# Kernel tuning notes

Hardware: AMD Instinct MI355X
Metric: run time of the kernel (lower is better)

Reference implementation:

```python
import jax, jax.numpy as jnp
import numpy as np


def setup_inputs() -> dict:
    key = jax.random.key(0)
    ks = jax.random.split(key, 5)
    B, C_in, C_out, H, W, k = 16, 64, 64, 256, 256, 16
    scale = 1.0 / (C_in * C_out)
    return {
        "u": jax.random.normal(ks[0], (B, C_in, H, W), dtype=jnp.float32),
        "W_pos_re": scale * jax.random.normal(ks[1], (C_in, C_out, k, k), dtype=jnp.float32),
        "W_pos_im": scale * jax.random.normal(ks[2], (C_in, C_out, k, k), dtype=jnp.float32),
        "W_neg_re": scale * jax.random.normal(ks[3], (C_in, C_out, k, k), dtype=jnp.float32),
        "W_neg_im": scale * jax.random.normal(ks[4], (C_in, C_out, k, k), dtype=jnp.float32),
    }


def reference(u, W_pos_re, W_pos_im, W_neg_re, W_neg_im):
    B, C_in, H, W = u.shape
    C_out = W_pos_re.shape[1]
    k = W_pos_re.shape[2]
    W_half = W // 2 + 1
    k_h = min(k, H // 2)
    k_w = min(k, W_half)

    R_pos = (W_pos_re + 1j * W_pos_im)[:, :, :k_h, :k_w]  # (C_in, C_out, k_h, k_w)
    R_neg = (W_neg_re + 1j * W_neg_im)[:, :, :k_h, :k_w]

    u_hat = jnp.fft.rfft2(u, norm="ortho")  # (B, C_in, H, W_half) complex

    # spectral multiply on retained modes only
    top = jnp.einsum("bchw,cohw->bohw", u_hat[:, :, :k_h, :k_w], R_pos)
    bot = jnp.einsum("bchw,cohw->bohw", u_hat[:, :, H - k_h:, :k_w], R_neg)

    v_hat = jnp.zeros((B, C_out, H, W_half), dtype=u_hat.dtype)
    v_hat = v_hat.at[:, :, :k_h, :k_w].set(top)
    v_hat = v_hat.at[:, :, H - k_h:, :k_w].set(bot)

    return jnp.fft.irfft2(v_hat, s=(H, W), norm="ortho")  # (B, C_out, H, W) real
```

## Files before the change

### kernel.cpp

```cpp
#include <hip/hip_runtime.h>


#define B_    16
#define H_    256
#define W_    256

#define OFF_CT 0
#define OFF_ST 256
#define OFF_RP 512
#define RP_SZ  (4096*512*2)
#define OFF_U  (OFF_RP + RP_SZ)
#define U_SZ   (512*1024*2)
#define OFF_V  (OFF_U + U_SZ)

#define UTP   260

typedef const __attribute__((address_space(1))) void g_void;
typedef __attribute__((address_space(3))) void l_void;

__device__ __forceinline__ void load_lds16(const float* g, float* l) {
    __builtin_amdgcn_global_load_lds((g_void*)g, (l_void*)l, 16, 0, 0);
}

__global__ void k_twiddle(float* __restrict__ ws) {
    int t = threadIdx.x;
    double a = 2.0 * 3.14159265358979323846 * (double)t / 256.0;
    ws[OFF_CT + t] = (float)cos(a);
    ws[OFF_ST + t] = (float)sin(a);
}

__global__ __launch_bounds__(256) void k_repack(const float* __restrict__ wpr,
                                                const float* __restrict__ wpi,
                                                const float* __restrict__ wnr,
                                                const float* __restrict__ wni,
                                                float* __restrict__ ws) {
    int co = blockIdx.x, t = threadIdx.x;
    int wm = t & 15;
    float norm = (wm == 0 ? 1.f : 2.f) * (1.f / 65536.f);
    size_t src = (size_t)co * 256 + t;
    float2* rp = (float2*)(ws + OFF_RP) + (size_t)co * 512;
    rp[t]       = make_float2(wpr[src] * norm, wpi[src] * norm);
    rp[t + 256] = make_float2(wnr[src] * norm, wni[src] * norm);
}

__global__ __launch_bounds__(256, 2) void k_fwd(const float* __restrict__ u,
                                                const float* __restrict__ ws,
                                                float* __restrict__ U) {
    __shared__ __align__(16) float ut[2][32][UTP];
    __shared__ __align__(16) float Pl[32][36];
    __shared__ float ct[256], st[256];
    int t = threadIdx.x, bc = blockIdx.x;
    ct[t] = ws[OFF_CT + t];
    st[t] = ws[OFF_ST + t];
    const float* ub = u + (size_t)bc * 65536;
    int lane = t & 63, w = t >> 6;
    int h = lane & 7, r8 = lane >> 3;
    int rowc = w * 8 + r8;

    #pragma unroll
    for (int k = 0; k < 8; ++k)
        load_lds16(ub + (w * 8 + k) * 256 + lane * 4, &ut[0][w * 8 + k][0]);
    #pragma unroll
    for (int k = 0; k < 8; ++k)
        load_lds16(ub + 8192 + (w * 8 + k) * 256 + lane * 4, &ut[1][w * 8 + k][0]);

    asm volatile("s_waitcnt lgkmcnt(0)" ::: "memory");
    __builtin_amdgcn_s_barrier();

    int wm0 = 2 * h, wm1 = wm0 + 1;
    float r0r = ct[wm0], r0i = -st[wm0];
    float r1r = ct[wm1], r1i = -st[wm1];
    float bs  = (h & 1) ? -1.f : 1.f;
    float dsg = (h & 1) ? 1.f : -1.f;

    int wm2 = t & 15, m1 = t >> 4;
    float q1r = ct[m1], q1i = -st[m1];
    int m2i = (16 - m1) & 255;
    float q2r = ct[m2i], q2i = st[m2i];
    float w1r = 1.f, w1i = 0.f, w2r = 1.f, w2i = 0.f;
    float U1r = 0.f, U1i = 0.f, U2r = 0.f, U2i = 0.f;

    for (int ch = 0; ch < 8; ++ch) {
        const int buf = ch & 1;
        if (ch < 7) asm volatile("s_waitcnt vmcnt(8)" ::: "memory");
        else        asm volatile("s_waitcnt vmcnt(0)" ::: "memory");

        float p0r = 0.f, p0i = 0.f, p1r = 0.f, p1i = 0.f;
        float t0r = 1.f, t0i = 0.f, t1r = 1.f, t1i = 0.f;
        const float* rowp = &ut[buf][rowc][0];
        #pragma unroll 4
        for (int bat = 0; bat < 16; ++bat) {
            const float* rp = rowp + 4 * bat;
            float4 q0 = *(const float4*)(rp);
            float4 q1 = *(const float4*)(rp + 64);
            float4 q2 = *(const float4*)(rp + 128);
            float4 q3 = *(const float4*)(rp + 192);
            #define PROC_(u0, u1, u2, u3) {                                   \
                float a_ = (u0) + (u2), b_ = (u1) + (u3);                     \
                float c_ = (u0) - (u2), d_ = (u1) - (u3);                     \
                float g0 = fmaf(bs, b_, a_);                                  \
                float g1r = c_, g1i = dsg * d_;                               \
                p0r = fmaf(g0, t0r, p0r);                                     \
                p0i = fmaf(g0, t0i, p0i);                                     \
                p1r = fmaf(g1r, t1r, fmaf(-g1i, t1i, p1r));                   \
                p1i = fmaf(g1r, t1i, fmaf( g1i, t1r, p1i));                   \
                float n0r = t0r * r0r - t0i * r0i;                            \
                float n0i = t0r * r0i + t0i * r0r;                            \
                float n1r = t1r * r1r - t1i * r1i;                            \
                float n1i = t1r * r1i + t1i * r1r;                            \
                t0r = n0r; t0i = n0i; t1r = n1r; t1i = n1i; }
            PROC_(q0.x, q1.x, q2.x, q3.x)
            PROC_(q0.y, q1.y, q2.y, q3.y)
            PROC_(q0.z, q1.z, q2.z, q3.z)
            PROC_(q0.w, q1.w, q2.w, q3.w)
            #undef PROC_
        }

        if (ch < 6) {
            const float* ub2 = ub + (ch + 2) * 8192;
            #pragma unroll
            for (int k = 0; k < 8; ++k)
                load_lds16(ub2 + (w * 8 + k) * 256 + lane * 4, &ut[buf][w * 8 + k][0]);
        }

        *(float4*)&Pl[rowc][4 * h] = make_float4(p0r, p0i, p1r, p1i);
        asm volatile("s_waitcnt lgkmcnt(0)" ::: "memory");
        __builtin_amdgcn_s_barrier();

        #pragma unroll 4
        for (int yy = 0; yy < 32; ++yy) {
            float2 g = *(float2*)&Pl[yy][2 * wm2];
            U1r = fmaf(g.x, w1r, fmaf(-g.y, w1i, U1r));
            U1i = fmaf(g.x, w1i, fmaf( g.y, w1r, U1i));
            U2r = fmaf(g.x, w2r, fmaf(-g.y, w2i, U2r));
            U2i = fmaf(g.x, w2i, fmaf( g.y, w2r, U2i));
            float n1r = w1r * q1r - w1i * q1i, n1i = w1r * q1i + w1i * q1r;
            float n2r = w2r * q2r - w2i * q2i, n2i = w2r * q2i + w2i * q2r;
            w1r = n1r; w1i = n1i; w2r = n2r; w2i = n2i;
        }
        __builtin_amdgcn_s_barrier();
    }

    float2* Ug = (float2*)U;
    Ug[(size_t)(m1 * 16 + wm2) * 1024 + bc]        = make_float2(U1r, U1i);
    Ug[(size_t)((m1 + 16) * 16 + wm2) * 1024 + bc] = make_float2(U2r, U2i);
}

__global__ __launch_bounds__(256) void k_cgemm(float* __restrict__ ws) {
    __shared__ float2 Ul[1024];
    int mw = blockIdx.x, t = threadIdx.x;
    const float2* Ug = (const float2*)(ws + OFF_U) + (size_t)mw * 1024;
    #pragma unroll
    for (int k = 0; k < 4; ++k) Ul[t + 256 * k] = Ug[t + 256 * k];
    __syncthreads();
    int o = t & 63, bq = t >> 6;
    const float2* rp = (const float2*)(ws + OFF_RP);
    float ar[4] = {0.f, 0.f, 0.f, 0.f}, ai[4] = {0.f, 0.f, 0.f, 0.f};
    #pragma unroll 4
    for (int c = 0; c < 64; ++c) {
        float2 R = rp[(size_t)(c * 64 + o) * 512 + mw];
        #pragma unroll
        for (int j = 0; j < 4; ++j) {
            float2 Uv = Ul[(bq * 4 + j) * 64 + c];
            ar[j] = fmaf(Uv.x, R.x, fmaf(-Uv.y, R.y, ar[j]));
            ai[j] = fmaf(Uv.x, R.y, fmaf( Uv.y, R.x, ai[j]));
        }
    }
    float2* Vg = (float2*)(ws + OFF_V);
    #pragma unroll
    for (int j = 0; j < 4; ++j)
        Vg[(size_t)((bq * 4 + j) * 64 + o) * 512 + mw] = make_float2(ar[j], ai[j]);
}

__global__ __launch_bounds__(256) void k_inv(const float* __restrict__ ws,
                                             float* __restrict__ out) {
    __shared__ float Vl[16][68];
    __shared__ float Tl[4][16][36];
    __shared__ float ct[256], st[256];
    int t = threadIdx.x;
    int bo = blockIdx.x >> 2, q = blockIdx.x & 3;
    ct[t] = ws[OFF_CT + t];
    st[t] = ws[OFF_ST + t];
    {
        const float2* Vg = (const float2*)(ws + OFF_V) + (size_t)bo * 512;
        float2 v0 = Vg[t];
        float2 v1 = Vg[t + 256];
        int m = t >> 4, wmv = t & 15;
        Vl[wmv][2 * m]        = v0.x;  Vl[wmv][2 * m + 1]        = v0.y;
        Vl[wmv][2 * (m + 16)] = v1.x;  Vl[wmv][2 * (m + 16) + 1] = v1.y;
    }
    __syncthreads();

    int wm4 = t & 15, yb = t >> 4;
    int y0 = q * 16 + yb;
    float vr[32], vi[32];
    #pragma unroll
    for (int m = 0; m < 32; ++m) { vr[m] = Vl[wm4][2 * m]; vi[m] = Vl[wm4][2 * m + 1]; }
    float cy = ct[y0], sy = st[y0];
    float T0r=0,T0i=0,T1r=0,T1i=0,T2r=0,T2i=0,T3r=0,T3i=0;
    float tr = 1.f, ti = 0.f;
    #pragma unroll
    for (int m = 0; m < 32; ++m) {
        if (m == 16) {
            int i16 = (4096 - 16 * y0) & 255;
            tr = ct[i16]; ti = st[i16];
        }
        float hr = vr[m] * tr - vi[m] * ti;
        float hi = vr[m] * ti + vi[m] * tr;
        const int md = m & 3;
        T0r += hr; T0i += hi;
        if (md == 0)      { T1r += hr; T1i += hi; T2r += hr; T2i += hi; T3r += hr; T3i += hi; }
        else if (md == 1) { T1r -= hi; T1i += hr; T2r -= hr; T2i -= hi; T3r += hi; T3i -= hr; }
        else if (md == 2) { T1r -= hr; T1i -= hi; T2r += hr; T2i += hi; T3r -= hr; T3i -= hi; }
        else              { T1r += hi; T1i -= hr; T2r -= hr; T2i -= hi; T3r -= hi; T3i += hr; }
        float nr = tr * cy - ti * sy, ni = tr * sy + ti * cy;
        tr = nr; ti = ni;
    }
    Tl[0][yb][wm4] = T0r; Tl[0][yb][16 + wm4] = T0i;
    Tl[1][yb][wm4] = T1r; Tl[1][yb][16 + wm4] = T1i;
    Tl[2][yb][wm4] = T2r; Tl[2][yb][16 + wm4] = T2i;
    Tl[3][yb][wm4] = T3r; Tl[3][yb][16 + wm4] = T3i;
    __syncthreads();

    int l = t & 63, wv = t >> 6;
    float c0[16], s0[16];
    #pragma unroll
    for (int wm = 0; wm < 16; ++wm) {
        int idx = (wm * l) & 255;
        c0[wm] = ct[idx]; s0[wm] = st[idx];
    }
    float* ob = out + (size_t)bo * 65536;
    for (int yi = 0; yi < 16; ++yi) {
        int y = wv * 64 + q * 16 + yi;
        float TR[16], TI[16];
        const float4* rowv = (const float4*)&Tl[wv][yi][0];
        #pragma unroll
        for (int qq = 0; qq < 4; ++qq) {
            float4 a = rowv[qq];
            TR[4*qq]=a.x; TR[4*qq+1]=a.y; TR[4*qq+2]=a.z; TR[4*qq+3]=a.w;
            float4 b = rowv[qq + 4];
            TI[4*qq]=b.x; TI[4*qq+1]=b.y; TI[4*qq+2]=b.z; TI[4*qq+3]=b.w;
        }
        #pragma unroll
        for (int k = 0; k < 4; ++k) {
            float a = 0.f;
            #pragma unroll
            for (int wm = 0; wm < 16; ++wm) {
                int p = (k * wm) & 3;
                if (p == 0)      a +=  TR[wm] * c0[wm] - TI[wm] * s0[wm];
                else if (p == 1) a += -TR[wm] * s0[wm] - TI[wm] * c0[wm];
                else if (p == 2) a += -TR[wm] * c0[wm] + TI[wm] * s0[wm];
                else             a +=  TR[wm] * s0[wm] + TI[wm] * c0[wm];
            }
            ob[(size_t)y * 256 + 64 * k + l] = a;
        }
    }
}

extern "C" void kernel_launch(void* const* d_in, const int* in_sizes, int n_in,
                              void* d_out, int out_size, void* d_ws, size_t ws_size,
                              hipStream_t stream) {
    const float* u   = (const float*)d_in[0];
    const float* wpr = (const float*)d_in[1];
    const float* wpi = (const float*)d_in[2];
    const float* wnr = (const float*)d_in[3];
    const float* wni = (const float*)d_in[4];
    float* out = (float*)d_out;
    float* ws  = (float*)d_ws;

    hipLaunchKernelGGL(k_twiddle, dim3(1),    dim3(256), 0, stream, ws);
    hipLaunchKernelGGL(k_repack,  dim3(4096), dim3(256), 0, stream, wpr, wpi, wnr, wni, ws);
    hipLaunchKernelGGL(k_fwd,     dim3(1024), dim3(256), 0, stream, u, ws, ws + OFF_U);
    hipLaunchKernelGGL(k_cgemm,   dim3(512),  dim3(256), 0, stream, ws);
    hipLaunchKernelGGL(k_inv,     dim3(4096), dim3(256), 0, stream, ws, out);
}
```

Baseline: 254.9 us.

## Single-buffer forward DFT tile, compute twiddles inline, fold twiddle kernel into repack

The forward row-DFT kernel now keeps one LDS tile instead of two. The next chunk is loaded after the current one is consumed, and the kernel waits on vmcnt(0) each iteration. Twiddles come from __sincosf instead of an LDS table loaded from workspace. The separate twiddle kernel is folded into block 0 of the repack kernel, saving one launch. Halving LDS and dropping the min-2-blocks launch bound may raise occupancy, but it removes the double-buffered prefetch overlap and uses lower-precision fast sincos.

```diff
diff --git a/kernel.cpp b/kernel.cpp
--- a/kernel.cpp
+++ b/kernel.cpp
@@ -14,19 +14,13 @@
 #define OFF_V  (OFF_U + U_SZ)
 
 #define UTP   260
+#define TWOPI_256 0.024543692606170259f
 
 typedef const __attribute__((address_space(1))) void g_void;
 typedef __attribute__((address_space(3))) void l_void;
 
 __device__ __forceinline__ void load_lds16(const float* g, float* l) {
     __builtin_amdgcn_global_load_lds((g_void*)g, (l_void*)l, 16, 0, 0);
-}
-
-__global__ void k_twiddle(float* __restrict__ ws) {
-    int t = threadIdx.x;
-    double a = 2.0 * 3.14159265358979323846 * (double)t / 256.0;
-    ws[OFF_CT + t] = (float)cos(a);
-    ws[OFF_ST + t] = (float)sin(a);
 }
 
 __global__ __launch_bounds__(256) void k_repack(const float* __restrict__ wpr,
@@ -35,6 +29,11 @@
                                                 const float* __restrict__ wni,
                                                 float* __restrict__ ws) {
     int co = blockIdx.x, t = threadIdx.x;
+    if (co == 0) {
+        double a = 2.0 * 3.14159265358979323846 * (double)t / 256.0;
+        ws[OFF_CT + t] = (float)cos(a);
+        ws[OFF_ST + t] = (float)sin(a);
+    }
     int wm = t & 15;
     float norm = (wm == 0 ? 1.f : 2.f) * (1.f / 65536.f);
     size_t src = (size_t)co * 256 + t;
@@ -43,51 +42,44 @@
     rp[t + 256] = make_float2(wnr[src] * norm, wni[src] * norm);
 }
 
-__global__ __launch_bounds__(256, 2) void k_fwd(const float* __restrict__ u,
-                                                const float* __restrict__ ws,
-                                                float* __restrict__ U) {
-    __shared__ __align__(16) float ut[2][32][UTP];
+__global__ __launch_bounds__(256) void k_fwd(const float* __restrict__ u,
+                                             float* __restrict__ U) {
+    __shared__ __align__(16) float ut[32][UTP];
     __shared__ __align__(16) float Pl[32][36];
-    __shared__ float ct[256], st[256];
     int t = threadIdx.x, bc = blockIdx.x;
-    ct[t] = ws[OFF_CT + t];
-    st[t] = ws[OFF_ST + t];
     const float* ub = u + (size_t)bc * 65536;
     int lane = t & 63, w = t >> 6;
+
+    #pragma unroll
+    for (int k = 0; k < 8; ++k)
+        load_lds16(ub + (w * 8 + k) * 256 + lane * 4, &ut[w * 8 + k][0]);
+
     int h = lane & 7, r8 = lane >> 3;
     int rowc = w * 8 + r8;
-
-    #pragma unroll
-    for (int k = 0; k < 8; ++k)
-        load_lds16(ub + (w * 8 + k) * 256 + lane * 4, &ut[0][w * 8 + k][0]);
-    #pragma unroll
-    for (int k = 0; k < 8; ++k)
-        load_lds16(ub + 8192 + (w * 8 + k) * 256 + lane * 4, &ut[1][w * 8 + k][0]);
-
-    asm volatile("s_waitcnt lgkmcnt(0)" ::: "memory");
-    __builtin_amdgcn_s_barrier();
-
     int wm0 = 2 * h, wm1 = wm0 + 1;
-    float r0r = ct[wm0], r0i = -st[wm0];
-    float r1r = ct[wm1], r1i = -st[wm1];
+    float s0v, c0v, s1v, c1v;
+    __sincosf(TWOPI_256 * (float)wm0, &s0v, &c0v);
+    __sincosf(TWOPI_256 * (float)wm1, &s1v, &c1v);
+    float r0r = c0v, r0i = -s0v;
+    float r1r = c1v, r1i = -s1v;
     float bs  = (h & 1) ? -1.f : 1.f;
     float dsg = (h & 1) ? 1.f : -1.f;
 
     int wm2 = t & 15, m1 = t >> 4;
-    float q1r = ct[m1], q1i = -st[m1];
-    int m2i = (16 - m1) & 255;
-    float q2r = ct[m2i], q2i = st[m2i];
+    float sv, cv;
+    __sincosf(TWOPI_256 * (float)m1, &sv, &cv);
+    float q1r = cv, q1i = -sv;
+    __sincosf(TWOPI_256 * (float)(m1 - 16), &sv, &cv);
+    float q2r = cv, q2i = -sv;
     float w1r = 1.f, w1i = 0.f, w2r = 1.f, w2i = 0.f;
     float U1r = 0.f, U1i = 0.f, U2r = 0.f, U2i = 0.f;
 
     for (int ch = 0; ch < 8; ++ch) {
-        const int buf = ch & 1;
-        if (ch < 7) asm volatile("s_waitcnt vmcnt(8)" ::: "memory");
-        else        asm volatile("s_waitcnt vmcnt(0)" ::: "memory");
+        asm volatile("s_waitcnt vmcnt(0)" ::: "memory");
 
         float p0r = 0.f, p0i = 0.f, p1r = 0.f, p1i = 0.f;
         float t0r = 1.f, t0i = 0.f, t1r = 1.f, t1i = 0.f;
-        const float* rowp = &ut[buf][rowc][0];
+        const float* rowp = &ut[rowc][0];
         #pragma unroll 4
         for (int bat = 0; bat < 16; ++bat) {
             const float* rp = rowp + 4 * bat;
@@ -116,11 +108,12 @@
             #undef PROC_
         }
 
-        if (ch < 6) {
-            const float* ub2 = ub + (ch + 2) * 8192;
+        __builtin_amdgcn_sched_barrier(0);
+        if (ch < 7) {
+            const float* ub2 = ub + (ch + 1) * 8192;
             #pragma unroll
             for (int k = 0; k < 8; ++k)
-                load_lds16(ub2 + (w * 8 + k) * 256 + lane * 4, &ut[buf][w * 8 + k][0]);
+                load_lds16(ub2 + (w * 8 + k) * 256 + lane * 4, &ut[w * 8 + k][0]);
         }
 
         *(float4*)&Pl[rowc][4 * h] = make_float4(p0r, p0i, p1r, p1i);
@@ -268,9 +261,8 @@
     float* out = (float*)d_out;
     float* ws  = (float*)d_ws;
 
-    hipLaunchKernelGGL(k_twiddle, dim3(1),    dim3(256), 0, stream, ws);
-    hipLaunchKernelGGL(k_repack,  dim3(4096), dim3(256), 0, stream, wpr, wpi, wnr, wni, ws);
-    hipLaunchKernelGGL(k_fwd,     dim3(1024), dim3(256), 0, stream, u, ws, ws + OFF_U);
-    hipLaunchKernelGGL(k_cgemm,   dim3(512),  dim3(256), 0, stream, ws);
-    hipLaunchKernelGGL(k_inv,     dim3(4096), dim3(256), 0, stream, ws, out);
-}
+    hipLaunchKernelGGL(k_repack, dim3(4096), dim3(256), 0, stream, wpr, wpi, wnr, wni, ws);
+    hipLaunchKernelGGL(k_fwd,    dim3(1024), dim3(256), 0, stream, u, ws + OFF_U);
+    hipLaunchKernelGGL(k_cgemm,  dim3(512),  dim3(256), 0, stream, ws);
+    hipLaunchKernelGGL(k_inv,    dim3(4096), dim3(256), 0, stream, ws, out);
+}
```

After: 247.0 us. 3.1% less time.
